# Performance work log

Hardware: AMD Instinct MI355X
Metric: run time of the kernel (lower is better)

The kernel has to match this reference:

```python
import jax, jax.numpy as jnp
import numpy as np

T = 1000
C = 3
H = 64
W = 64
N_ITER = 3  # fixed-point iterations standing in for the DEQ solver


def _make_coeffs():
    # DDIM coefficient precompute, mirroring get_ddim_injection with sddim=False
    betas = np.linspace(1e-4, 0.02, T, dtype=np.float64)
    # compute_alpha prepends beta_0 = 0, so alphabar has length T+1 with alphabar[0]=1
    alphabar = np.cumprod(np.concatenate([[1.0], 1.0 - betas]))
    t = np.arange(T - 1, -1, -1)            # cur_seq[::-1] = [T-1, ..., 0]
    at = alphabar[t + 1]                    # alphabar indexed at t+1
    at_next = alphabar[t]                   # next_t = t-1  ->  alphabar[next_t+1]
    alpha_ratio = np.sqrt(at_next / at[0])
    et_coeff2 = np.sqrt(1.0 - at_next) - np.sqrt((1.0 - at) * at_next / at)
    et_coeff = et_coeff2 / np.sqrt(at_next)
    et_prevsum_coeff = np.sqrt(at_next)
    rs = lambda a: jnp.asarray(a.reshape(T, 1, 1, 1), dtype=jnp.float32)
    return rs(alpha_ratio), rs(et_coeff), rs(et_prevsum_coeff), jnp.asarray(t, dtype=jnp.int32)


def setup_inputs() -> dict:
    key = jax.random.key(0)
    k1, k2, k3 = jax.random.split(key, 3)
    alpha_ratio, et_coeff, et_prevsum_coeff, t = _make_coeffs()
    x = jax.random.normal(k1, (T + 1, C, H, W), dtype=jnp.float32)
    conv_w = jax.random.normal(k2, (C, C, 3, 3), dtype=jnp.float32) * 0.1
    temb = jax.random.normal(k3, (T, C), dtype=jnp.float32) * 0.1
    return {"x": x, "t": t, "alpha_ratio": alpha_ratio, "et_coeff": et_coeff,
            "et_prevsum_coeff": et_prevsum_coeff, "conv_w": conv_w, "temb": temb}


def _model(xt_in, t, conv_w, temb):
    # epsilon model stand-in: 3x3 conv + per-timestep channel bias
    y = jax.lax.conv_general_dilated(
        xt_in, conv_w, window_strides=(1, 1), padding="SAME",
        dimension_numbers=("NCHW", "OIHW", "NCHW"))
    return y + temb[t][:, :, None, None]


def reference(x, t, alpha_ratio, et_coeff, et_prevsum_coeff, conv_w, temb):
    xT = x[0:1]                                   # [1,C,H,W]
    all_xT = alpha_ratio * xT                     # broadcast == repeat_interleave then scale -> [T,C,H,W]

    def func(xt):
        xt_in = xt[:T]                            # gather via next_idx = [0..T-1]
        et = _model(xt_in, t, conv_w, temb)
        et_updated = et_coeff * et
        et_prevsum = jnp.cumsum(et_updated, axis=0)
        xt_next = all_xT + et_prevsum_coeff * et_prevsum
        # scatter: xt_all[xT_idx]=xT, xt_all[prev_idx]=xt_next  (xT_idx=[0], prev_idx=[1..T])
        return jnp.concatenate([xT, xt_next], axis=0)

    xt = x
    for _ in range(N_ITER):
        xt = func(xt)
    return xt
```

## Files before the change

kernel.cpp:

```cpp
#include <hip/hip_runtime.h>
#include <hip/hip_bf16.h>

#define TT 1000
#define CC 3
#define HH 64
#define WW 64
#define HW 4096
#define CHW 12288
#define CHW4 3072
#define NCHUNK 50
#define CLEN 20

__device__ __forceinline__ float bf2f(unsigned short u) {
    return __uint_as_float(((unsigned)u) << 16);
}
__device__ __forceinline__ unsigned short f2bf(float f) {
    unsigned u = __float_as_uint(f);
    return (unsigned short)((u + 0x7FFFu + ((u >> 16) & 1u)) >> 16);
}

__global__ __launch_bounds__(256) void copy_xT_kernel(const float4* __restrict__ x,
                                                      float4* __restrict__ out,
                                                      unsigned short* __restrict__ X) {
    int i = blockIdx.x * 256 + threadIdx.x;
    if (i < CHW4) {
        float4 v = x[i];
        out[i] = v;
        ushort4 u;
        u.x = f2bf(v.x); u.y = f2bf(v.y); u.z = f2bf(v.z); u.w = f2bf(v.w);
        *(ushort4*)(X + i * 4) = u;
    }
}

template <bool IN_BF16>
__global__ __launch_bounds__(256) void conv_kernel(const void* __restrict__ xin_v,
                                                   const float* __restrict__ cw,
                                                   const float* __restrict__ temb,
                                                   const int* __restrict__ tarr,
                                                   const float* __restrict__ ec,
                                                   unsigned short* __restrict__ A) {
    int idx = blockIdx.x * 256 + threadIdx.x;
    int wi = idx & 15;
    int hp = (idx >> 4) & 31;
    int t  = idx >> 9;
    int h0 = hp * 2;
    int w0 = wi * 4;

    const float* xtf = (const float*)xin_v + (size_t)t * CHW;
    const unsigned short* xtb = (const unsigned short*)xin_v + (size_t)t * CHW;

    float acc[2][CC][4];
    #pragma unroll
    for (int o = 0; o < 2; ++o)
        #pragma unroll
        for (int co = 0; co < CC; ++co)
            #pragma unroll
            for (int k = 0; k < 4; ++k) acc[o][co][k] = 0.f;

    #pragma unroll
    for (int ch = 0; ch < CC; ++ch) {
        #pragma unroll
        for (int j = 0; j < 4; ++j) {
            int h = h0 - 1 + j;
            bool hv = (unsigned)h < (unsigned)HH;
            float4 M;
            if (IN_BF16) {
                ushort4 u = make_ushort4(0, 0, 0, 0);
                if (hv) u = *(const ushort4*)(xtb + ch * HW + h * WW + w0);
                M = make_float4(bf2f(u.x), bf2f(u.y), bf2f(u.z), bf2f(u.w));
            } else {
                M = hv ? *(const float4*)(xtf + ch * HW + h * WW + w0)
                       : make_float4(0.f, 0.f, 0.f, 0.f);
            }
            float left  = __shfl_up(M.w, 1);    if (wi == 0)  left  = 0.f;
            float right = __shfl_down(M.x, 1);  if (wi == 15) right = 0.f;
            float win[6] = {left, M.x, M.y, M.z, M.w, right};
            #pragma unroll
            for (int o = 0; o < 2; ++o) {
                const int kh = j - o;
                if (kh >= 0 && kh <= 2) {
                    #pragma unroll
                    for (int co = 0; co < CC; ++co) {
                        float wa = cw[((co * CC + ch) * 3 + kh) * 3 + 0];
                        float wb = cw[((co * CC + ch) * 3 + kh) * 3 + 1];
                        float wc = cw[((co * CC + ch) * 3 + kh) * 3 + 2];
                        #pragma unroll
                        for (int k = 0; k < 4; ++k)
                            acc[o][co][k] += win[k] * wa + win[k + 1] * wb + win[k + 2] * wc;
                    }
                }
            }
        }
    }

    float e = ec[t];
    int tr = tarr[t];
    #pragma unroll
    for (int o = 0; o < 2; ++o)
        #pragma unroll
        for (int co = 0; co < CC; ++co) {
            float b = temb[tr * CC + co];
            ushort4 v;
            v.x = f2bf(e * (acc[o][co][0] + b));
            v.y = f2bf(e * (acc[o][co][1] + b));
            v.z = f2bf(e * (acc[o][co][2] + b));
            v.w = f2bf(e * (acc[o][co][3] + b));
            *(ushort4*)(A + (size_t)t * CHW + co * HW + (h0 + o) * WW + w0) = v;
        }
}

__global__ __launch_bounds__(256) void chunk_sum_kernel(const unsigned short* __restrict__ A,
                                                        float4* __restrict__ S) {
    int ch = blockIdx.x / 12;
    int pos4 = (blockIdx.x % 12) * 256 + threadIdx.x;
    const unsigned short* p = A + (size_t)ch * CLEN * CHW + pos4 * 4;
    float4 acc = make_float4(0.f, 0.f, 0.f, 0.f);
    #pragma unroll
    for (int i = 0; i < CLEN; ++i) {
        ushort4 u = *(const ushort4*)(p + (size_t)i * CHW);
        acc.x += bf2f(u.x); acc.y += bf2f(u.y); acc.z += bf2f(u.z); acc.w += bf2f(u.w);
    }
    S[(size_t)ch * CHW4 + pos4] = acc;
}

__global__ __launch_bounds__(256) void offset_scan_kernel(float4* __restrict__ S) {
    int pos4 = blockIdx.x * 256 + threadIdx.x;
    if (pos4 >= CHW4) return;
    float4 run = make_float4(0.f, 0.f, 0.f, 0.f);
    #pragma unroll
    for (int ch = 0; ch < NCHUNK; ++ch) {
        float4 v = S[ch * CHW4 + pos4];
        S[ch * CHW4 + pos4] = run;
        run.x += v.x; run.y += v.y; run.z += v.z; run.w += v.w;
    }
}

template <bool OUT_BF16>
__global__ __launch_bounds__(256) void final_kernel(const unsigned short* __restrict__ A,
                                                    const float4* __restrict__ S,
                                                    const float4* __restrict__ xT,
                                                    const float* __restrict__ ar,
                                                    const float* __restrict__ epc,
                                                    void* __restrict__ out_v) {
    int ch = blockIdx.x / 12;
    int pos4 = (blockIdx.x % 12) * 256 + threadIdx.x;
    float4 acc = S[(size_t)ch * CHW4 + pos4];
    float4 xv = xT[pos4];
    const unsigned short* p = A + (size_t)ch * CLEN * CHW + pos4 * 4;
    float4* qf = (float4*)out_v + (size_t)(ch * CLEN + 1) * CHW4 + pos4;
    unsigned short* qb = (unsigned short*)out_v + ((size_t)(ch * CLEN + 1) * CHW4 + pos4) * 4;
    #pragma unroll
    for (int i = 0; i < CLEN; ++i) {
        int t = ch * CLEN + i;
        ushort4 u = *(const ushort4*)(p + (size_t)i * CHW);
        acc.x += bf2f(u.x); acc.y += bf2f(u.y); acc.z += bf2f(u.z); acc.w += bf2f(u.w);
        float a = ar[t], e = epc[t];
        float4 r = make_float4(a * xv.x + e * acc.x, a * xv.y + e * acc.y,
                               a * xv.z + e * acc.z, a * xv.w + e * acc.w);
        if (OUT_BF16) {
            ushort4 ub;
            ub.x = f2bf(r.x); ub.y = f2bf(r.y); ub.z = f2bf(r.z); ub.w = f2bf(r.w);
            *(ushort4*)(qb + (size_t)i * CHW) = ub;
        } else {
            qf[(size_t)i * CHW4] = r;
        }
    }
}

extern "C" void kernel_launch(void* const* d_in, const int* in_sizes, int n_in,
                              void* d_out, int out_size, void* d_ws, size_t ws_size,
                              hipStream_t stream) {
    const float* x    = (const float*)d_in[0];
    const int*   tarr = (const int*)  d_in[1];
    const float* ar   = (const float*)d_in[2];
    const float* ec   = (const float*)d_in[3];
    const float* epc  = (const float*)d_in[4];
    const float* cw   = (const float*)d_in[5];
    const float* temb = (const float*)d_in[6];
    float* out = (float*)d_out;

    unsigned short* A = (unsigned short*)d_ws;
    float* S = (float*)(A + (size_t)TT * CHW);
    unsigned short* X = (unsigned short*)(S + (size_t)NCHUNK * CHW);

    copy_xT_kernel<<<12, 256, 0, stream>>>((const float4*)x, (float4*)out, X);

    conv_kernel<false><<<2000, 256, 0, stream>>>(x, cw, temb, tarr, ec, A);
    chunk_sum_kernel<<<NCHUNK * 12, 256, 0, stream>>>(A, (float4*)S);
    offset_scan_kernel<<<12, 256, 0, stream>>>((float4*)S);
    final_kernel<true><<<NCHUNK * 12, 256, 0, stream>>>(A, (const float4*)S,
                                                        (const float4*)x, ar, epc, X);

    conv_kernel<true><<<2000, 256, 0, stream>>>(X, cw, temb, tarr, ec, A);
    chunk_sum_kernel<<<NCHUNK * 12, 256, 0, stream>>>(A, (float4*)S);
    offset_scan_kernel<<<12, 256, 0, stream>>>((float4*)S);
    final_kernel<true><<<NCHUNK * 12, 256, 0, stream>>>(A, (const float4*)S,
                                                        (const float4*)x, ar, epc, X);

    conv_kernel<true><<<2000, 256, 0, stream>>>(X, cw, temb, tarr, ec, A);
    chunk_sum_kernel<<<NCHUNK * 12, 256, 0, stream>>>(A, (float4*)S);
    offset_scan_kernel<<<12, 256, 0, stream>>>((float4*)S);
    final_kernel<false><<<NCHUNK * 12, 256, 0, stream>>>(A, (const float4*)S,
                                                         (const float4*)x, ar, epc, out);
}
```

Measured before the change: 209.1 us.

## Fuse state reconstruction, conv and chunk sums into one kernel per iteration

```diff
diff --git a/kernel.cpp b/kernel.cpp
--- a/kernel.cpp
+++ b/kernel.cpp
@@ -1,5 +1,4 @@
 #include <hip/hip_runtime.h>
-#include <hip/hip_bf16.h>
 
 #define TT 1000
 #define CC 3
@@ -8,8 +7,9 @@
 #define HW 4096
 #define CHW 12288
 #define CHW4 3072
-#define NCHUNK 50
-#define CLEN 20
+#define NCHUNK 250
+#define CLEN 4
+#define WP 68
 
 __device__ __forceinline__ float bf2f(unsigned short u) {
     return __uint_as_float(((unsigned)u) << 16);
@@ -19,151 +19,282 @@
     return (unsigned short)((u + 0x7FFFu + ((u >> 16) & 1u)) >> 16);
 }
 
-__global__ __launch_bounds__(256) void copy_xT_kernel(const float4* __restrict__ x,
-                                                      float4* __restrict__ out,
-                                                      unsigned short* __restrict__ X) {
+__global__ __launch_bounds__(256) void copy_out0_kernel(const float4* __restrict__ x,
+                                                        float4* __restrict__ out) {
     int i = blockIdx.x * 256 + threadIdx.x;
-    if (i < CHW4) {
-        float4 v = x[i];
-        out[i] = v;
-        ushort4 u;
-        u.x = f2bf(v.x); u.y = f2bf(v.y); u.z = f2bf(v.z); u.w = f2bf(v.w);
-        *(ushort4*)(X + i * 4) = u;
-    }
-}
-
-template <bool IN_BF16>
-__global__ __launch_bounds__(256) void conv_kernel(const void* __restrict__ xin_v,
-                                                   const float* __restrict__ cw,
-                                                   const float* __restrict__ temb,
-                                                   const int* __restrict__ tarr,
-                                                   const float* __restrict__ ec,
-                                                   unsigned short* __restrict__ A) {
-    int idx = blockIdx.x * 256 + threadIdx.x;
-    int wi = idx & 15;
-    int hp = (idx >> 4) & 31;
-    int t  = idx >> 9;
-    int h0 = hp * 2;
-    int w0 = wi * 4;
-
-    const float* xtf = (const float*)xin_v + (size_t)t * CHW;
-    const unsigned short* xtb = (const unsigned short*)xin_v + (size_t)t * CHW;
-
-    float acc[2][CC][4];
-    #pragma unroll
-    for (int o = 0; o < 2; ++o)
+    if (i < CHW4) out[i] = x[i];
+}
+
+__global__ __launch_bounds__(1024) void conv1_kernel(const float* __restrict__ x,
+                                                     const float* __restrict__ cw,
+                                                     const float* __restrict__ temb,
+                                                     const int* __restrict__ tarr,
+                                                     const float* __restrict__ ec,
+                                                     unsigned short* __restrict__ Aout,
+                                                     float* __restrict__ S) {
+    __shared__ float st[CC][HH][WP];
+    int tid = threadIdx.x;
+    int w4 = tid & 15;
+    int h  = tid >> 4;
+    int w0 = w4 * 4;
+    int c  = blockIdx.x;
+    int t0 = c * CLEN;
+
+    float sum[CC][4];
+    #pragma unroll
+    for (int co = 0; co < CC; ++co)
+        #pragma unroll
+        for (int k = 0; k < 4; ++k) sum[co][k] = 0.f;
+
+    #pragma unroll
+    for (int i = 0; i < CLEN; ++i) {
+        int t = t0 + i;
+        float4 m[CC];
+        #pragma unroll
+        for (int ch = 0; ch < CC; ++ch)
+            m[ch] = *(const float4*)(x + (size_t)t * CHW + ch * HW + h * WW + w0);
+        if (i > 0) __syncthreads();
+        #pragma unroll
+        for (int ch = 0; ch < CC; ++ch)
+            *(float4*)&st[ch][h][w0] = m[ch];
+        __syncthreads();
+
+        float acc[CC][4];
         #pragma unroll
         for (int co = 0; co < CC; ++co)
             #pragma unroll
-            for (int k = 0; k < 4; ++k) acc[o][co][k] = 0.f;
-
-    #pragma unroll
-    for (int ch = 0; ch < CC; ++ch) {
-        #pragma unroll
-        for (int j = 0; j < 4; ++j) {
-            int h = h0 - 1 + j;
-            bool hv = (unsigned)h < (unsigned)HH;
-            float4 M;
-            if (IN_BF16) {
-                ushort4 u = make_ushort4(0, 0, 0, 0);
-                if (hv) u = *(const ushort4*)(xtb + ch * HW + h * WW + w0);
-                M = make_float4(bf2f(u.x), bf2f(u.y), bf2f(u.z), bf2f(u.w));
-            } else {
-                M = hv ? *(const float4*)(xtf + ch * HW + h * WW + w0)
-                       : make_float4(0.f, 0.f, 0.f, 0.f);
-            }
-            float left  = __shfl_up(M.w, 1);    if (wi == 0)  left  = 0.f;
-            float right = __shfl_down(M.x, 1);  if (wi == 15) right = 0.f;
-            float win[6] = {left, M.x, M.y, M.z, M.w, right};
-            #pragma unroll
-            for (int o = 0; o < 2; ++o) {
-                const int kh = j - o;
-                if (kh >= 0 && kh <= 2) {
+            for (int k = 0; k < 4; ++k) acc[co][k] = 0.f;
+
+        #pragma unroll
+        for (int ch = 0; ch < CC; ++ch) {
+            #pragma unroll
+            for (int dh = 0; dh < 3; ++dh) {
+                int r = h - 1 + dh;
+                float4 M = make_float4(0.f, 0.f, 0.f, 0.f);
+                if ((unsigned)r < (unsigned)HH) M = *(const float4*)&st[ch][r][w0];
+                float left  = __shfl_up(M.w, 1);   if (w4 == 0)  left  = 0.f;
+                float right = __shfl_down(M.x, 1); if (w4 == 15) right = 0.f;
+                float win[6] = {left, M.x, M.y, M.z, M.w, right};
+                #pragma unroll
+                for (int co = 0; co < CC; ++co) {
+                    float wa = cw[((co * CC + ch) * 3 + dh) * 3 + 0];
+                    float wb = cw[((co * CC + ch) * 3 + dh) * 3 + 1];
+                    float wc = cw[((co * CC + ch) * 3 + dh) * 3 + 2];
                     #pragma unroll
-                    for (int co = 0; co < CC; ++co) {
-                        float wa = cw[((co * CC + ch) * 3 + kh) * 3 + 0];
-                        float wb = cw[((co * CC + ch) * 3 + kh) * 3 + 1];
-                        float wc = cw[((co * CC + ch) * 3 + kh) * 3 + 2];
-                        #pragma unroll
-                        for (int k = 0; k < 4; ++k)
-                            acc[o][co][k] += win[k] * wa + win[k + 1] * wb + win[k + 2] * wc;
-                    }
+                    for (int k = 0; k < 4; ++k)
+                        acc[co][k] += win[k] * wa + win[k + 1] * wb + win[k + 2] * wc;
                 }
             }
         }
-    }
-
-    float e = ec[t];
-    int tr = tarr[t];
-    #pragma unroll
-    for (int o = 0; o < 2; ++o)
+
+        float e = ec[t];
+        int tr = tarr[t];
         #pragma unroll
         for (int co = 0; co < CC; ++co) {
             float b = temb[tr * CC + co];
-            ushort4 v;
-            v.x = f2bf(e * (acc[o][co][0] + b));
-            v.y = f2bf(e * (acc[o][co][1] + b));
-            v.z = f2bf(e * (acc[o][co][2] + b));
-            v.w = f2bf(e * (acc[o][co][3] + b));
-            *(ushort4*)(A + (size_t)t * CHW + co * HW + (h0 + o) * WW + w0) = v;
-        }
-}
-
-__global__ __launch_bounds__(256) void chunk_sum_kernel(const unsigned short* __restrict__ A,
-                                                        float4* __restrict__ S) {
-    int ch = blockIdx.x / 12;
-    int pos4 = (blockIdx.x % 12) * 256 + threadIdx.x;
-    const unsigned short* p = A + (size_t)ch * CLEN * CHW + pos4 * 4;
-    float4 acc = make_float4(0.f, 0.f, 0.f, 0.f);
+            ushort4 u;
+            u.x = f2bf(e * (acc[co][0] + b));
+            u.y = f2bf(e * (acc[co][1] + b));
+            u.z = f2bf(e * (acc[co][2] + b));
+            u.w = f2bf(e * (acc[co][3] + b));
+            *(ushort4*)(Aout + (size_t)t * CHW + co * HW + h * WW + w0) = u;
+            sum[co][0] += bf2f(u.x); sum[co][1] += bf2f(u.y);
+            sum[co][2] += bf2f(u.z); sum[co][3] += bf2f(u.w);
+        }
+    }
+
+    #pragma unroll
+    for (int co = 0; co < CC; ++co)
+        *(float4*)(S + (size_t)c * CHW + co * HW + h * WW + w0) =
+            make_float4(sum[co][0], sum[co][1], sum[co][2], sum[co][3]);
+}
+
+__global__ __launch_bounds__(1024) void fused_kernel(const unsigned short* __restrict__ Ain,
+                                                     const float* __restrict__ x,
+                                                     float* __restrict__ S,
+                                                     unsigned short* __restrict__ Aout,
+                                                     const float* __restrict__ cw,
+                                                     const float* __restrict__ temb,
+                                                     const int* __restrict__ tarr,
+                                                     const float* __restrict__ ec,
+                                                     const float* __restrict__ ar,
+                                                     const float* __restrict__ epc) {
+    __shared__ unsigned short st[CC][HH][WP];
+    int tid = threadIdx.x;
+    int w4 = tid & 15;
+    int h  = tid >> 4;
+    int w0 = w4 * 4;
+    int c  = blockIdx.x;
+    int t0 = c * CLEN;
+
+    float xT[CC][4], run[CC][4], state[CC][4], sum[CC][4];
+    #pragma unroll
+    for (int ch = 0; ch < CC; ++ch) {
+        int off = ch * HW + h * WW + w0;
+        float4 xv = *(const float4*)(x + off);
+        float4 rv = *(const float4*)(S + (size_t)c * CHW + off);
+        xT[ch][0] = xv.x; xT[ch][1] = xv.y; xT[ch][2] = xv.z; xT[ch][3] = xv.w;
+        run[ch][0] = rv.x; run[ch][1] = rv.y; run[ch][2] = rv.z; run[ch][3] = rv.w;
+        #pragma unroll
+        for (int k = 0; k < 4; ++k) sum[ch][k] = 0.f;
+    }
+
+    if (c == 0) {
+        #pragma unroll
+        for (int ch = 0; ch < CC; ++ch)
+            #pragma unroll
+            for (int k = 0; k < 4; ++k) state[ch][k] = xT[ch][k];
+    } else {
+        float a = ar[t0 - 1], p = epc[t0 - 1];
+        #pragma unroll
+        for (int ch = 0; ch < CC; ++ch)
+            #pragma unroll
+            for (int k = 0; k < 4; ++k)
+                state[ch][k] = a * xT[ch][k] + p * run[ch][k];
+    }
+    #pragma unroll
+    for (int ch = 0; ch < CC; ++ch) {
+        ushort4 u;
+        u.x = f2bf(state[ch][0]); u.y = f2bf(state[ch][1]);
+        u.z = f2bf(state[ch][2]); u.w = f2bf(state[ch][3]);
+        *(ushort4*)&st[ch][h][w0] = u;
+    }
+    __syncthreads();
+
     #pragma unroll
     for (int i = 0; i < CLEN; ++i) {
-        ushort4 u = *(const ushort4*)(p + (size_t)i * CHW);
-        acc.x += bf2f(u.x); acc.y += bf2f(u.y); acc.z += bf2f(u.z); acc.w += bf2f(u.w);
-    }
-    S[(size_t)ch * CHW4 + pos4] = acc;
-}
-
-__global__ __launch_bounds__(256) void offset_scan_kernel(float4* __restrict__ S) {
-    int pos4 = blockIdx.x * 256 + threadIdx.x;
-    if (pos4 >= CHW4) return;
-    float4 run = make_float4(0.f, 0.f, 0.f, 0.f);
-    #pragma unroll
-    for (int ch = 0; ch < NCHUNK; ++ch) {
-        float4 v = S[ch * CHW4 + pos4];
-        S[ch * CHW4 + pos4] = run;
-        run.x += v.x; run.y += v.y; run.z += v.z; run.w += v.w;
-    }
-}
-
-template <bool OUT_BF16>
+        int t = t0 + i;
+
+        ushort4 av[CC];
+        if (i < CLEN - 1) {
+            #pragma unroll
+            for (int ch = 0; ch < CC; ++ch)
+                av[ch] = *(const ushort4*)(Ain + (size_t)t * CHW + ch * HW + h * WW + w0);
+        }
+
+        float acc[CC][4];
+        #pragma unroll
+        for (int co = 0; co < CC; ++co)
+            #pragma unroll
+            for (int k = 0; k < 4; ++k) acc[co][k] = 0.f;
+
+        #pragma unroll
+        for (int ch = 0; ch < CC; ++ch) {
+            #pragma unroll
+            for (int dh = 0; dh < 3; ++dh) {
+                int r = h - 1 + dh;
+                float4 M = make_float4(0.f, 0.f, 0.f, 0.f);
+                if ((unsigned)r < (unsigned)HH) {
+                    ushort4 u = *(const ushort4*)&st[ch][r][w0];
+                    M = make_float4(bf2f(u.x), bf2f(u.y), bf2f(u.z), bf2f(u.w));
+                }
+                float left  = __shfl_up(M.w, 1);   if (w4 == 0)  left  = 0.f;
+                float right = __shfl_down(M.x, 1); if (w4 == 15) right = 0.f;
+                float win[6] = {left, M.x, M.y, M.z, M.w, right};
+                #pragma unroll
+                for (int co = 0; co < CC; ++co) {
+                    float wa = cw[((co * CC + ch) * 3 + dh) * 3 + 0];
+                    float wb = cw[((co * CC + ch) * 3 + dh) * 3 + 1];
+                    float wc = cw[((co * CC + ch) * 3 + dh) * 3 + 2];
+                    #pragma unroll
+                    for (int k = 0; k < 4; ++k)
+                        acc[co][k] += win[k] * wa + win[k + 1] * wb + win[k + 2] * wc;
+                }
+            }
+        }
+
+        float e = ec[t];
+        int tr = tarr[t];
+        #pragma unroll
+        for (int co = 0; co < CC; ++co) {
+            float b = temb[tr * CC + co];
+            ushort4 u;
+            u.x = f2bf(e * (acc[co][0] + b));
+            u.y = f2bf(e * (acc[co][1] + b));
+            u.z = f2bf(e * (acc[co][2] + b));
+            u.w = f2bf(e * (acc[co][3] + b));
+            *(ushort4*)(Aout + (size_t)t * CHW + co * HW + h * WW + w0) = u;
+            sum[co][0] += bf2f(u.x); sum[co][1] += bf2f(u.y);
+            sum[co][2] += bf2f(u.z); sum[co][3] += bf2f(u.w);
+        }
+
+        if (i < CLEN - 1) {
+            float a = ar[t], p = epc[t];
+            #pragma unroll
+            for (int ch = 0; ch < CC; ++ch) {
+                run[ch][0] += bf2f(av[ch].x); run[ch][1] += bf2f(av[ch].y);
+                run[ch][2] += bf2f(av[ch].z); run[ch][3] += bf2f(av[ch].w);
+                #pragma unroll
+                for (int k = 0; k < 4; ++k)
+                    state[ch][k] = a * xT[ch][k] + p * run[ch][k];
+            }
+            __syncthreads();
+            #pragma unroll
+            for (int ch = 0; ch < CC; ++ch) {
+                ushort4 u;
+                u.x = f2bf(state[ch][0]); u.y = f2bf(state[ch][1]);
+                u.z = f2bf(state[ch][2]); u.w = f2bf(state[ch][3]);
+                *(ushort4*)&st[ch][h][w0] = u;
+            }
+            __syncthreads();
+        }
+    }
+
+    #pragma unroll
+    for (int co = 0; co < CC; ++co)
+        *(float4*)(S + (size_t)c * CHW + co * HW + h * WW + w0) =
+            make_float4(sum[co][0], sum[co][1], sum[co][2], sum[co][3]);
+}
+
+__global__ __launch_bounds__(256) void scan_kernel(float4* __restrict__ S) {
+    int gid  = blockIdx.x * 256 + threadIdx.x;
+    int wid  = gid >> 6;
+    int lane = threadIdx.x & 63;
+    float4 carry = make_float4(0.f, 0.f, 0.f, 0.f);
+    #pragma unroll
+    for (int seg = 0; seg < (NCHUNK + 63) / 64; ++seg) {
+        int cc = seg * 64 + lane;
+        float4 v = make_float4(0.f, 0.f, 0.f, 0.f);
+        if (cc < NCHUNK) v = S[(size_t)cc * CHW4 + wid];
+        float4 incl = v;
+        #pragma unroll
+        for (int d = 1; d < 64; d <<= 1) {
+            float tx = __shfl_up(incl.x, d), ty = __shfl_up(incl.y, d);
+            float tz = __shfl_up(incl.z, d), tw = __shfl_up(incl.w, d);
+            if (lane >= d) { incl.x += tx; incl.y += ty; incl.z += tz; incl.w += tw; }
+        }
+        float4 ex;
+        ex.x = __shfl_up(incl.x, 1); ex.y = __shfl_up(incl.y, 1);
+        ex.z = __shfl_up(incl.z, 1); ex.w = __shfl_up(incl.w, 1);
+        if (lane == 0) ex = make_float4(0.f, 0.f, 0.f, 0.f);
+        if (cc < NCHUNK)
+            S[(size_t)cc * CHW4 + wid] = make_float4(carry.x + ex.x, carry.y + ex.y,
+                                                     carry.z + ex.z, carry.w + ex.w);
+        carry.x += __shfl(incl.x, 63); carry.y += __shfl(incl.y, 63);
+        carry.z += __shfl(incl.z, 63); carry.w += __shfl(incl.w, 63);
+    }
+}
+
 __global__ __launch_bounds__(256) void final_kernel(const unsigned short* __restrict__ A,
                                                     const float4* __restrict__ S,
                                                     const float4* __restrict__ xT,
                                                     const float* __restrict__ ar,
                                                     const float* __restrict__ epc,
-                                                    void* __restrict__ out_v) {
+                                                    float4* __restrict__ out) {
     int ch = blockIdx.x / 12;
     int pos4 = (blockIdx.x % 12) * 256 + threadIdx.x;
     float4 acc = S[(size_t)ch * CHW4 + pos4];
     float4 xv = xT[pos4];
     const unsigned short* p = A + (size_t)ch * CLEN * CHW + pos4 * 4;
-    float4* qf = (float4*)out_v + (size_t)(ch * CLEN + 1) * CHW4 + pos4;
-    unsigned short* qb = (unsigned short*)out_v + ((size_t)(ch * CLEN + 1) * CHW4 + pos4) * 4;
+    float4* qf = out + (size_t)(ch * CLEN + 1) * CHW4 + pos4;
     #pragma unroll
     for (int i = 0; i < CLEN; ++i) {
         int t = ch * CLEN + i;
         ushort4 u = *(const ushort4*)(p + (size_t)i * CHW);
         acc.x += bf2f(u.x); acc.y += bf2f(u.y); acc.z += bf2f(u.z); acc.w += bf2f(u.w);
         float a = ar[t], e = epc[t];
-        float4 r = make_float4(a * xv.x + e * acc.x, a * xv.y + e * acc.y,
-                               a * xv.z + e * acc.z, a * xv.w + e * acc.w);
-        if (OUT_BF16) {
-            ushort4 ub;
-            ub.x = f2bf(r.x); ub.y = f2bf(r.y); ub.z = f2bf(r.z); ub.w = f2bf(r.w);
-            *(ushort4*)(qb + (size_t)i * CHW) = ub;
-        } else {
-            qf[(size_t)i * CHW4] = r;
-        }
+        qf[(size_t)i * CHW4] = make_float4(a * xv.x + e * acc.x, a * xv.y + e * acc.y,
+                                           a * xv.z + e * acc.z, a * xv.w + e * acc.w);
     }
 }
 
@@ -179,27 +310,20 @@
     const float* temb = (const float*)d_in[6];
     float* out = (float*)d_out;
 
-    unsigned short* A = (unsigned short*)d_ws;
-    float* S = (float*)(A + (size_t)TT * CHW);
-    unsigned short* X = (unsigned short*)(S + (size_t)NCHUNK * CHW);
-
-    copy_xT_kernel<<<12, 256, 0, stream>>>((const float4*)x, (float4*)out, X);
-
-    conv_kernel<false><<<2000, 256, 0, stream>>>(x, cw, temb, tarr, ec, A);
-    chunk_sum_kernel<<<NCHUNK * 12, 256, 0, stream>>>(A, (float4*)S);
-    offset_scan_kernel<<<12, 256, 0, stream>>>((float4*)S);
-    final_kernel<true><<<NCHUNK * 12, 256, 0, stream>>>(A, (const float4*)S,
-                                                        (const float4*)x, ar, epc, X);
-
-    conv_kernel<true><<<2000, 256, 0, stream>>>(X, cw, temb, tarr, ec, A);
-    chunk_sum_kernel<<<NCHUNK * 12, 256, 0, stream>>>(A, (float4*)S);
-    offset_scan_kernel<<<12, 256, 0, stream>>>((float4*)S);
-    final_kernel<true><<<NCHUNK * 12, 256, 0, stream>>>(A, (const float4*)S,
-                                                        (const float4*)x, ar, epc, X);
-
-    conv_kernel<true><<<2000, 256, 0, stream>>>(X, cw, temb, tarr, ec, A);
-    chunk_sum_kernel<<<NCHUNK * 12, 256, 0, stream>>>(A, (float4*)S);
-    offset_scan_kernel<<<12, 256, 0, stream>>>((float4*)S);
-    final_kernel<false><<<NCHUNK * 12, 256, 0, stream>>>(A, (const float4*)S,
-                                                         (const float4*)x, ar, epc, out);
-}
+    unsigned short* A1 = (unsigned short*)d_ws;
+    unsigned short* A2 = A1 + (size_t)TT * CHW;
+    float* S = (float*)(A2 + (size_t)TT * CHW);
+
+    copy_out0_kernel<<<12, 256, 0, stream>>>((const float4*)x, (float4*)out);
+
+    conv1_kernel<<<NCHUNK, 1024, 0, stream>>>(x, cw, temb, tarr, ec, A1, S);
+    scan_kernel<<<768, 256, 0, stream>>>((float4*)S);
+
+    fused_kernel<<<NCHUNK, 1024, 0, stream>>>(A1, x, S, A2, cw, temb, tarr, ec, ar, epc);
+    scan_kernel<<<768, 256, 0, stream>>>((float4*)S);
+    fused_kernel<<<NCHUNK, 1024, 0, stream>>>(A2, x, S, A1, cw, temb, tarr, ec, ar, epc);
+    scan_kernel<<<768, 256, 0, stream>>>((float4*)S);
+
+    final_kernel<<<NCHUNK * 12, 256, 0, stream>>>(A1, (const float4*)S,
+                                                  (const float4*)x, ar, epc, (float4*)out);
+}
```

After: 233.3 us. 11.6% more time.

## Parallelize chunk-offset scan across wavefronts, double chunks, fold xT copy into conv

Applied to the files above, without the earlier changes.

```diff
diff --git a/kernel.cpp b/kernel.cpp
--- a/kernel.cpp
+++ b/kernel.cpp
@@ -1,5 +1,4 @@
 #include <hip/hip_runtime.h>
-#include <hip/hip_bf16.h>
 
 #define TT 1000
 #define CC 3
@@ -8,8 +7,9 @@
 #define HW 4096
 #define CHW 12288
 #define CHW4 3072
-#define NCHUNK 50
-#define CLEN 20
+#define NCHUNK 100
+#define CLEN 10
+#define NCONVB 2000
 
 __device__ __forceinline__ float bf2f(unsigned short u) {
     return __uint_as_float(((unsigned)u) << 16);
@@ -19,26 +19,27 @@
     return (unsigned short)((u + 0x7FFFu + ((u >> 16) & 1u)) >> 16);
 }
 
-__global__ __launch_bounds__(256) void copy_xT_kernel(const float4* __restrict__ x,
-                                                      float4* __restrict__ out,
-                                                      unsigned short* __restrict__ X) {
-    int i = blockIdx.x * 256 + threadIdx.x;
-    if (i < CHW4) {
-        float4 v = x[i];
-        out[i] = v;
-        ushort4 u;
-        u.x = f2bf(v.x); u.y = f2bf(v.y); u.z = f2bf(v.z); u.w = f2bf(v.w);
-        *(ushort4*)(X + i * 4) = u;
-    }
-}
-
-template <bool IN_BF16>
+template <bool IN_BF16, bool COPY_TAIL>
 __global__ __launch_bounds__(256) void conv_kernel(const void* __restrict__ xin_v,
                                                    const float* __restrict__ cw,
                                                    const float* __restrict__ temb,
                                                    const int* __restrict__ tarr,
                                                    const float* __restrict__ ec,
-                                                   unsigned short* __restrict__ A) {
+                                                   unsigned short* __restrict__ A,
+                                                   float* __restrict__ out0,
+                                                   unsigned short* __restrict__ X0) {
+    if (COPY_TAIL && blockIdx.x >= NCONVB) {
+        int i = (blockIdx.x - NCONVB) * 256 + threadIdx.x;
+        if (i < CHW4) {
+            float4 v = ((const float4*)xin_v)[i];
+            ((float4*)out0)[i] = v;
+            ushort4 u;
+            u.x = f2bf(v.x); u.y = f2bf(v.y); u.z = f2bf(v.z); u.w = f2bf(v.w);
+            *(ushort4*)(X0 + (size_t)i * 4) = u;
+        }
+        return;
+    }
+
     int idx = blockIdx.x * 256 + threadIdx.x;
     int wi = idx & 15;
     int hp = (idx >> 4) & 31;
@@ -123,15 +124,32 @@
     S[(size_t)ch * CHW4 + pos4] = acc;
 }
 
-__global__ __launch_bounds__(256) void offset_scan_kernel(float4* __restrict__ S) {
-    int pos4 = blockIdx.x * 256 + threadIdx.x;
-    if (pos4 >= CHW4) return;
-    float4 run = make_float4(0.f, 0.f, 0.f, 0.f);
-    #pragma unroll
-    for (int ch = 0; ch < NCHUNK; ++ch) {
-        float4 v = S[ch * CHW4 + pos4];
-        S[ch * CHW4 + pos4] = run;
-        run.x += v.x; run.y += v.y; run.z += v.z; run.w += v.w;
+__global__ __launch_bounds__(256) void scan_kernel(float4* __restrict__ S) {
+    int gid  = blockIdx.x * 256 + threadIdx.x;
+    int wid  = gid >> 6;
+    int lane = threadIdx.x & 63;
+    float4 carry = make_float4(0.f, 0.f, 0.f, 0.f);
+    #pragma unroll
+    for (int seg = 0; seg < (NCHUNK + 63) / 64; ++seg) {
+        int cc = seg * 64 + lane;
+        float4 v = make_float4(0.f, 0.f, 0.f, 0.f);
+        if (cc < NCHUNK) v = S[(size_t)cc * CHW4 + wid];
+        float4 incl = v;
+        #pragma unroll
+        for (int d = 1; d < 64; d <<= 1) {
+            float tx = __shfl_up(incl.x, d), ty = __shfl_up(incl.y, d);
+            float tz = __shfl_up(incl.z, d), tw = __shfl_up(incl.w, d);
+            if (lane >= d) { incl.x += tx; incl.y += ty; incl.z += tz; incl.w += tw; }
+        }
+        float4 ex;
+        ex.x = __shfl_up(incl.x, 1); ex.y = __shfl_up(incl.y, 1);
+        ex.z = __shfl_up(incl.z, 1); ex.w = __shfl_up(incl.w, 1);
+        if (lane == 0) ex = make_float4(0.f, 0.f, 0.f, 0.f);
+        if (cc < NCHUNK)
+            S[(size_t)cc * CHW4 + wid] = make_float4(carry.x + ex.x, carry.y + ex.y,
+                                                     carry.z + ex.z, carry.w + ex.w);
+        carry.x += __shfl(incl.x, 63); carry.y += __shfl(incl.y, 63);
+        carry.z += __shfl(incl.z, 63); carry.w += __shfl(incl.w, 63);
     }
 }
 
@@ -183,23 +201,21 @@
     float* S = (float*)(A + (size_t)TT * CHW);
     unsigned short* X = (unsigned short*)(S + (size_t)NCHUNK * CHW);
 
-    copy_xT_kernel<<<12, 256, 0, stream>>>((const float4*)x, (float4*)out, X);
-
-    conv_kernel<false><<<2000, 256, 0, stream>>>(x, cw, temb, tarr, ec, A);
+    conv_kernel<false, true><<<NCONVB + 12, 256, 0, stream>>>(x, cw, temb, tarr, ec, A, out, X);
     chunk_sum_kernel<<<NCHUNK * 12, 256, 0, stream>>>(A, (float4*)S);
-    offset_scan_kernel<<<12, 256, 0, stream>>>((float4*)S);
+    scan_kernel<<<768, 256, 0, stream>>>((float4*)S);
     final_kernel<true><<<NCHUNK * 12, 256, 0, stream>>>(A, (const float4*)S,
                                                         (const float4*)x, ar, epc, X);
 
-    conv_kernel<true><<<2000, 256, 0, stream>>>(X, cw, temb, tarr, ec, A);
+    conv_kernel<true, false><<<NCONVB, 256, 0, stream>>>(X, cw, temb, tarr, ec, A, out, X);
     chunk_sum_kernel<<<NCHUNK * 12, 256, 0, stream>>>(A, (float4*)S);
-    offset_scan_kernel<<<12, 256, 0, stream>>>((float4*)S);
+    scan_kernel<<<768, 256, 0, stream>>>((float4*)S);
     final_kernel<true><<<NCHUNK * 12, 256, 0, stream>>>(A, (const float4*)S,
                                                         (const float4*)x, ar, epc, X);
 
-    conv_kernel<true><<<2000, 256, 0, stream>>>(X, cw, temb, tarr, ec, A);
+    conv_kernel<true, false><<<NCONVB, 256, 0, stream>>>(X, cw, temb, tarr, ec, A, out, X);
     chunk_sum_kernel<<<NCHUNK * 12, 256, 0, stream>>>(A, (float4*)S);
-    offset_scan_kernel<<<12, 256, 0, stream>>>((float4*)S);
+    scan_kernel<<<768, 256, 0, stream>>>((float4*)S);
     final_kernel<false><<<NCHUNK * 12, 256, 0, stream>>>(A, (const float4*)S,
                                                          (const float4*)x, ar, epc, out);
 }
```

New measurement: 213.0 us. No clear change (+1.9%).
